# Performance work log

Hardware: AMD Instinct MI355X
Metric: run time of the kernel (lower is better)

The kernel has to match this reference:

```python
import jax, jax.numpy as jnp
import numpy as np

B_, T_, L_, M_, H_, F_ = 16, 2048, 128, 256, 512, 1024
EPS = 1e-5


def _init_reservoir(h, rng):
    # orthogonal matrix scaled inside the unit disk for a stable linear recurrence
    q, _ = np.linalg.qr(rng.standard_normal((h, h)).astype(np.float32))
    return jnp.asarray(0.95 * q, dtype=jnp.float32)


def setup_inputs() -> dict:
    key = jax.random.key(0)
    ks = jax.random.split(key, 8)
    rng = np.random.default_rng(0)
    s = lambda fan_in: 1.0 / np.sqrt(fan_in)
    return {
        "x": jax.random.normal(ks[0], (B_, T_, L_), dtype=jnp.float32),
        "We": jax.random.uniform(ks[1], (L_, M_), jnp.float32, -s(L_), s(L_)),
        "be": jnp.zeros((M_,), jnp.float32),
        "Wb": jax.random.uniform(ks[2], (M_, H_), jnp.float32, -s(M_), s(M_)),
        "A": _init_reservoir(H_, rng),
        "Wr": jax.random.uniform(ks[3], (L_, H_), jnp.float32, -s(L_), s(L_)),
        "br": jnp.zeros((H_,), jnp.float32),
        "ln_g": jnp.ones((H_,), jnp.float32),
        "ln_b": jnp.zeros((H_,), jnp.float32),
        "W1": jax.random.uniform(ks[4], (H_, F_), jnp.float32, -s(H_), s(H_)),
        "b1": jnp.zeros((F_,), jnp.float32),
        "W2": jax.random.uniform(ks[5], (F_, H_), jnp.float32, -s(F_), s(F_)),
        "b2": jnp.zeros((H_,), jnp.float32),
    }


def reference(x, We, be, Wb, A, Wr, br, ln_g, ln_b, W1, b1, W2, b2):
    # encoder + B projection, batched over all timesteps: [B,T,H]
    Bu = (x @ We + be) @ Wb

    # sequential linear recurrence h_t = h_{t-1} @ A + Bu_t, h_0 = Bu_0
    def step(h, bu_t):
        h = h @ A + bu_t
        return h, h

    h0 = jnp.zeros((x.shape[0], A.shape[0]), x.dtype)
    _, Hs = jax.lax.scan(step, h0, jnp.swapaxes(Bu, 0, 1))  # [T,B,H]
    H_seq = jnp.swapaxes(Hs, 0, 1)  # [B,T,H]

    # residual + layer norm
    z = H_seq + (x @ Wr + br)
    mu = jnp.mean(z, axis=-1, keepdims=True)
    var = jnp.mean(jnp.square(z - mu), axis=-1, keepdims=True)
    zn = (z - mu) * jax.lax.rsqrt(var + EPS) * ln_g + ln_b

    # MLP on last timestep
    h_last = zn[:, -1, :]
    out = jax.nn.relu(h_last @ W1 + b1) @ W2 + b2
    return out
```

## Files before the change

### kernel.cpp

```cpp
#include <hip/hip_runtime.h>

#define B_  16
#define T_  2048
#define L_  128
#define M_  256
#define H_  512
#define F_  1024
#define EPS 1e-5f

#define LDA_S 36
#define LDB_S 68
#define SMSZ (64 * LDA_S + 64 * LDB_S)

__device__ __forceinline__ float4 load_a4(const float* __restrict__ A,
                                          const float* __restrict__ Alast,
                                          int M, int lda, int amode,
                                          int gr, int gk) {
    float4 av = make_float4(0.f, 0.f, 0.f, 0.f);
    if (gr < M) {
        const float* p;
        if (amode == 1)
            p = A + (long)((gr & 15) * T_ + (T_ - 1 - (gr >> 4))) * L_ + gk;
        else if (amode == 2)
            p = A + (long)(((gr >> 4) << 5) + 16 + (gr & 15)) * lda + gk;
        else if (amode == 3 && gr == M - 1)
            p = Alast + gk;
        else
            p = A + (long)gr * lda + gk;
        av = *(const float4*)p;
    }
    return av;
}

__device__ __forceinline__ void gemm_tile(
    float* sm,
    const float* __restrict__ A, const float* __restrict__ Alast,
    const float* __restrict__ Bm, const float* __restrict__ bias,
    const float* __restrict__ Add, float* __restrict__ C,
    int M, int K, int lda, int ldb, int ldc,
    int flags, int amode, int bx, int by)
{
    constexpr int BM = 32, BN = 64, BK = 64, TM = 2, TN = 4;
    float* As = sm;
    float* Bs = sm + BK * LDA_S;
    const int tid = threadIdx.x;
    const int tx = tid & 15;
    const int ty = tid >> 4;
    const int row0 = by * BM, col0 = bx * BN;

    float4 pa[2], pb[4];
#pragma unroll
    for (int t = 0; t < 2; ++t) {
        int f = tid + t * 256;
        pa[t] = load_a4(A, Alast, M, lda, amode, row0 + (f >> 4), (f & 15) * 4);
    }
#pragma unroll
    for (int t = 0; t < 4; ++t) {
        int f = tid + t * 256;
        pb[t] = *(const float4*)(Bm + (long)(f >> 4) * ldb + col0 + (f & 15) * 4);
    }

    float acc[TM][TN] = {};

    for (int k0 = 0; k0 < K; k0 += BK) {
        __syncthreads();
#pragma unroll
        for (int t = 0; t < 2; ++t) {
            int f = tid + t * 256;
            int arow = f >> 4, kk = (f & 15) * 4;
            As[(kk + 0) * LDA_S + arow] = pa[t].x;
            As[(kk + 1) * LDA_S + arow] = pa[t].y;
            As[(kk + 2) * LDA_S + arow] = pa[t].z;
            As[(kk + 3) * LDA_S + arow] = pa[t].w;
        }
#pragma unroll
        for (int t = 0; t < 4; ++t) {
            int f = tid + t * 256;
            *(float4*)&Bs[(f >> 4) * LDB_S + (f & 15) * 4] = pb[t];
        }
        __syncthreads();
        int kn = k0 + BK;
        if (kn < K) {
#pragma unroll
            for (int t = 0; t < 2; ++t) {
                int f = tid + t * 256;
                pa[t] = load_a4(A, Alast, M, lda, amode, row0 + (f >> 4), kn + (f & 15) * 4);
            }
#pragma unroll
            for (int t = 0; t < 4; ++t) {
                int f = tid + t * 256;
                pb[t] = *(const float4*)(Bm + (long)(kn + (f >> 4)) * ldb + col0 + (f & 15) * 4);
            }
        }
#pragma unroll
        for (int kk = 0; kk < BK; ++kk) {
            float ra[TM], rb[TN];
#pragma unroll
            for (int i = 0; i < TM; ++i) ra[i] = As[kk * LDA_S + ty * TM + i];
#pragma unroll
            for (int j = 0; j < TN; ++j) rb[j] = Bs[kk * LDB_S + tx * TN + j];
#pragma unroll
            for (int i = 0; i < TM; ++i)
#pragma unroll
                for (int j = 0; j < TN; ++j)
                    acc[i][j] = fmaf(ra[i], rb[j], acc[i][j]);
        }
    }

#pragma unroll
    for (int i = 0; i < TM; ++i) {
        int r = row0 + ty * TM + i;
        if (r >= M) continue;
#pragma unroll
        for (int j = 0; j < TN; ++j) {
            int c = col0 + tx * TN + j;
            float v = acc[i][j];
            if (flags & 1) v += bias[c];
            if (amode == 2) v += Add[(long)(((r >> 4) << 5) + (r & 15)) * ldc + c];
            C[(long)r * ldc + c] = v;
        }
    }
}

__global__ __launch_bounds__(256) void dual(
    const float* A, const float* Alast, const float* Bm, const float* bias,
    const float* Add, float* C, int M, int K, int lda, int ldb, int ldc,
    int flags, int amode, int nbxA, int nA,
    const float* SqL, const float* SqR, float* SqOut)
{
    __shared__ float sm[SMSZ];
    int j = blockIdx.x;
    if (j < nA)
        gemm_tile(sm, A, Alast, Bm, bias, Add, C, M, K, lda, ldb, ldc,
                  flags, amode, j % nbxA, j / nbxA);
    else {
        int s = j - nA;
        gemm_tile(sm, SqL, nullptr, SqR, nullptr, nullptr, SqOut,
                  H_, H_, H_, H_, H_, 0, 0, s % 8, s / 8);
    }
}

#define TLDA 20
#define TLDB 68
#define TSM (64 * TLDA + 64 * TLDB)

__device__ __forceinline__ float4 z_a4(const float* __restrict__ V1,
                                       const float* __restrict__ x,
                                       int b, int gk) {
    int seg = gk >> 9;
    if (seg < 3)
        return *(const float4*)(V1 + (long)((seg + 1) * 16 + b) * H_ + (gk & 511));
    return *(const float4*)(x + ((long)b * T_ + (T_ - 1)) * L_ + (gk - 1536));
}

__device__ __forceinline__ float4 z_b4(const float* __restrict__ P32,
                                       const float* __restrict__ P64,
                                       const float* __restrict__ P96,
                                       const float* __restrict__ Wr,
                                       int kr, int c) {
    const float* p;
    if (kr < 512)       p = P32 + (long)kr * H_;
    else if (kr < 1024) p = P64 + (long)(kr - 512) * H_;
    else if (kr < 1536) p = P96 + (long)(kr - 1024) * H_;
    else                p = Wr + (long)(kr - 1536) * H_;
    return *(const float4*)(p + c);
}

__global__ __launch_bounds__(256) void zpart(
    const float* __restrict__ V1, const float* __restrict__ x,
    const float* __restrict__ P32, const float* __restrict__ P64,
    const float* __restrict__ P96, const float* __restrict__ Wr,
    float* __restrict__ zp)
{
    __shared__ float sm[TSM];
    float* As = sm;
    float* Bs = sm + 64 * TLDA;
    const int tid = threadIdx.x;
    const int tx = tid & 15, ty = tid >> 4;
    const int kc = blockIdx.x >> 3;
    const int col0 = (blockIdx.x & 7) * 64;
    const int kOff = kc * 128;

    float4 pa, pb[4];
    pa = z_a4(V1, x, tid >> 4, kOff + (tid & 15) * 4);
#pragma unroll
    for (int t = 0; t < 4; ++t) {
        int f = tid + t * 256;
        pb[t] = z_b4(P32, P64, P96, Wr, kOff + (f >> 4), col0 + (f & 15) * 4);
    }

    float acc[4] = {};
    for (int k0 = kOff; k0 < kOff + 128; k0 += 64) {
        __syncthreads();
        {
            int arow = tid >> 4, kk = (tid & 15) * 4;
            As[(kk + 0) * TLDA + arow] = pa.x;
            As[(kk + 1) * TLDA + arow] = pa.y;
            As[(kk + 2) * TLDA + arow] = pa.z;
            As[(kk + 3) * TLDA + arow] = pa.w;
        }
#pragma unroll
        for (int t = 0; t < 4; ++t) {
            int f = tid + t * 256;
            *(float4*)&Bs[(f >> 4) * TLDB + (f & 15) * 4] = pb[t];
        }
        __syncthreads();
        int kn = k0 + 64;
        if (kn < kOff + 128) {
            pa = z_a4(V1, x, tid >> 4, kn + (tid & 15) * 4);
#pragma unroll
            for (int t = 0; t < 4; ++t) {
                int f = tid + t * 256;
                pb[t] = z_b4(P32, P64, P96, Wr, kn + (f >> 4), col0 + (f & 15) * 4);
            }
        }
#pragma unroll
        for (int kk = 0; kk < 64; ++kk) {
            float ra = As[kk * TLDA + ty];
            float4 rb = *(float4*)&Bs[kk * TLDB + tx * 4];
            acc[0] = fmaf(ra, rb.x, acc[0]);
            acc[1] = fmaf(ra, rb.y, acc[1]);
            acc[2] = fmaf(ra, rb.z, acc[2]);
            acc[3] = fmaf(ra, rb.w, acc[3]);
        }
    }

    float* dst = zp + (long)kc * 16 * H_ + (long)ty * H_ + col0 + tx * 4;
    *(float4*)dst = make_float4(acc[0], acc[1], acc[2], acc[3]);
}

__global__ __launch_bounds__(256) void mlp1z(
    const float* __restrict__ V1, const float* __restrict__ zp,
    const float* __restrict__ br, const float* __restrict__ lng,
    const float* __restrict__ lnb, const float* __restrict__ W1,
    const float* __restrict__ b1, float* __restrict__ hid)
{
    __shared__ float znL[16 * 512];
    __shared__ float Bs[64 * TLDB];
    const int tid = threadIdx.x;

    {
        const int r = tid >> 4;
        const int l = tid & 15;
        float4 zv[8];
        float s1 = 0.f, s2 = 0.f;
#pragma unroll
        for (int i = 0; i < 8; ++i) {
            int c = l * 4 + i * 64;
            float4 v = *(const float4*)(V1 + (long)r * H_ + c);
            float4 bb = *(const float4*)(br + c);
            v.x += bb.x; v.y += bb.y; v.z += bb.z; v.w += bb.w;
#pragma unroll
            for (int kc = 0; kc < 13; ++kc) {
                float4 p = *(const float4*)(zp + (long)kc * 16 * H_ + (long)r * H_ + c);
                v.x += p.x; v.y += p.y; v.z += p.z; v.w += p.w;
            }
            zv[i] = v;
            s1 += v.x + v.y + v.z + v.w;
            s2 += v.x * v.x + v.y * v.y + v.z * v.z + v.w * v.w;
        }
#pragma unroll
        for (int off = 1; off < 16; off <<= 1) {
            s1 += __shfl_xor(s1, off, 64);
            s2 += __shfl_xor(s2, off, 64);
        }
        float mu  = s1 * (1.0f / H_);
        float var = s2 * (1.0f / H_) - mu * mu;
        float rs  = rsqrtf(var + EPS);
#pragma unroll
        for (int i = 0; i < 8; ++i) {
            int c = l * 4 + i * 64;
            float4 g  = *(const float4*)(lng + c);
            float4 bt = *(const float4*)(lnb + c);
            float4 v  = zv[i];
            v.x = (v.x - mu) * rs * g.x + bt.x;
            v.y = (v.y - mu) * rs * g.y + bt.y;
            v.z = (v.z - mu) * rs * g.z + bt.z;
            v.w = (v.w - mu) * rs * g.w + bt.w;
            *(float4*)&znL[r * 512 + c] = v;
        }
    }
    __syncthreads();

    const int tx = tid & 15, ty = tid >> 4;
    const int col0 = blockIdx.x * 64;

    float4 pb[4];
#pragma unroll
    for (int t = 0; t < 4; ++t) {
        int f = tid + t * 256;
        pb[t] = *(const float4*)(W1 + (long)(f >> 4) * F_ + col0 + (f & 15) * 4);
    }
    float acc[4] = {};
    for (int k0 = 0; k0 < H_; k0 += 64) {
        __syncthreads();
#pragma unroll
        for (int t = 0; t < 4; ++t) {
            int f = tid + t * 256;
            *(float4*)&Bs[(f >> 4) * TLDB + (f & 15) * 4] = pb[t];
        }
        __syncthreads();
        int kn = k0 + 64;
        if (kn < H_) {
#pragma unroll
            for (int t = 0; t < 4; ++t) {
                int f = tid + t * 256;
                pb[t] = *(const float4*)(W1 + (long)(kn + (f >> 4)) * F_ + col0 + (f & 15) * 4);
            }
        }
#pragma unroll
        for (int kk = 0; kk < 64; ++kk) {
            float ra = znL[ty * 512 + k0 + kk];
            float4 rb = *(float4*)&Bs[kk * TLDB + tx * 4];
            acc[0] = fmaf(ra, rb.x, acc[0]);
            acc[1] = fmaf(ra, rb.y, acc[1]);
            acc[2] = fmaf(ra, rb.z, acc[2]);
            acc[3] = fmaf(ra, rb.w, acc[3]);
        }
    }
    int c = col0 + tx * 4;
    float4 v;
    v.x = fmaxf(acc[0] + b1[c + 0], 0.f);
    v.y = fmaxf(acc[1] + b1[c + 1], 0.f);
    v.z = fmaxf(acc[2] + b1[c + 2], 0.f);
    v.w = fmaxf(acc[3] + b1[c + 3], 0.f);
    *(float4*)(hid + (long)ty * F_ + c) = v;
}

__global__ __launch_bounds__(256) void mlp2k(
    const float* __restrict__ hid, const float* __restrict__ W2,
    const float* __restrict__ b2, float* __restrict__ out)
{
    __shared__ float sm[TSM];
    float* As = sm;
    float* Bs = sm + 64 * TLDA;
    const int tid = threadIdx.x;
    const int tx = tid & 15, ty = tid >> 4;
    const int col0 = blockIdx.x * 64;

    float4 pa, pb[4];
    pa = *(const float4*)(hid + (long)(tid >> 4) * F_ + (tid & 15) * 4);
#pragma unroll
    for (int t = 0; t < 4; ++t) {
        int f = tid + t * 256;
        pb[t] = *(const float4*)(W2 + (long)(f >> 4) * H_ + col0 + (f & 15) * 4);
    }

    float acc[4] = {};
    for (int k0 = 0; k0 < F_; k0 += 64) {
        __syncthreads();
        {
            int arow = tid >> 4, kk = (tid & 15) * 4;
            As[(kk + 0) * TLDA + arow] = pa.x;
            As[(kk + 1) * TLDA + arow] = pa.y;
            As[(kk + 2) * TLDA + arow] = pa.z;
            As[(kk + 3) * TLDA + arow] = pa.w;
        }
#pragma unroll
        for (int t = 0; t < 4; ++t) {
            int f = tid + t * 256;
            *(float4*)&Bs[(f >> 4) * TLDB + (f & 15) * 4] = pb[t];
        }
        __syncthreads();
        int kn = k0 + 64;
        if (kn < F_) {
            pa = *(const float4*)(hid + (long)(tid >> 4) * F_ + kn + (tid & 15) * 4);
#pragma unroll
            for (int t = 0; t < 4; ++t) {
                int f = tid + t * 256;
                pb[t] = *(const float4*)(W2 + (long)(kn + (f >> 4)) * H_ + col0 + (f & 15) * 4);
            }
        }
#pragma unroll
        for (int kk = 0; kk < 64; ++kk) {
            float ra = As[kk * TLDA + ty];
            float4 rb = *(float4*)&Bs[kk * TLDB + tx * 4];
            acc[0] = fmaf(ra, rb.x, acc[0]);
            acc[1] = fmaf(ra, rb.y, acc[1]);
            acc[2] = fmaf(ra, rb.z, acc[2]);
            acc[3] = fmaf(ra, rb.w, acc[3]);
        }
    }

    int c = col0 + tx * 4;
    float4 v;
    v.x = acc[0] + b2[c + 0];
    v.y = acc[1] + b2[c + 1];
    v.z = acc[2] + b2[c + 2];
    v.w = acc[3] + b2[c + 3];
    *(float4*)(out + (long)ty * H_ + c) = v;
}

extern "C" void kernel_launch(void* const* d_in, const int* in_sizes, int n_in,
                              void* d_out, int out_size, void* d_ws, size_t ws_size,
                              hipStream_t stream) {
    const float* x    = (const float*)d_in[0];
    const float* We   = (const float*)d_in[1];
    const float* be   = (const float*)d_in[2];
    const float* Wb   = (const float*)d_in[3];
    const float* Amat = (const float*)d_in[4];
    const float* Wr   = (const float*)d_in[5];
    const float* br   = (const float*)d_in[6];
    const float* lng  = (const float*)d_in[7];
    const float* lnb  = (const float*)d_in[8];
    const float* W1   = (const float*)d_in[9];
    const float* b1   = (const float*)d_in[10];
    const float* W2   = (const float*)d_in[11];
    const float* b2   = (const float*)d_in[12];
    float* out = (float*)d_out;

    float* ws  = (float*)d_ws;
    float* Wc  = ws;
    float* V0  = Wc + 129 * H_;
    float* V1  = V0 + 2048 * H_;
    float* P2  = V1 + 1024 * H_;
    float* P4  = P2 + H_ * H_;
    float* P8  = P4 + H_ * H_;
    float* P16 = P8 + H_ * H_;
    float* P32 = P16 + H_ * H_;
    float* P64 = P32 + H_ * H_;
    float* P96 = P64 + H_ * H_;
    float* hid = P96 + H_ * H_;
    float* zp  = hid + B_ * F_;

    dual<<<168, 256, 0, stream>>>(We, be, Wb, nullptr, nullptr, Wc,
                                  129, M_, M_, H_, H_, 0, 3, 8, 40,
                                  Amat, Amat, P2);
    dual<<<640, 256, 0, stream>>>(x, nullptr, Wc, Wc + 128 * H_, nullptr, V0,
                                  2048, L_, L_, H_, H_, 1, 1, 8, 512,
                                  P2, P2, P4);
    dual<<<384, 256, 0, stream>>>(V0, nullptr, Amat, nullptr, V0, V1,
                                  1024, H_, H_, H_, H_, 0, 2, 8, 256,
                                  P4, P4, P8);
    dual<<<256, 256, 0, stream>>>(V1, nullptr, P2, nullptr, V1, V0,
                                  512, H_, H_, H_, H_, 0, 2, 8, 128,
                                  P8, P8, P16);
    dual<<<192, 256, 0, stream>>>(V0, nullptr, P4, nullptr, V0, V1,
                                  256, H_, H_, H_, H_, 0, 2, 8, 64,
                                  P16, P16, P32);
    dual<<<160, 256, 0, stream>>>(V1, nullptr, P8, nullptr, V1, V0,
                                  128, H_, H_, H_, H_, 0, 2, 8, 32,
                                  P32, P32, P64);
    dual<<<144, 256, 0, stream>>>(V0, nullptr, P16, nullptr, V0, V1,
                                  64, H_, H_, H_, H_, 0, 2, 8, 16,
                                  P32, P64, P96);
    zpart<<<104, 256, 0, stream>>>(V1, x, P32, P64, P96, Wr, zp);
    mlp1z<<<16, 256, 0, stream>>>(V1, zp, br, lng, lnb, W1, b1, hid);
    mlp2k<<<8, 256, 0, stream>>>(hid, W2, b2, out);
}
```

Measured before the change: 326.9 us.

## Split-K the final MLP GEMMs across more blocks with a reduction kernel

The two MLP matmuls on the last timestep previously ran on 16 and 8 blocks with long K loops. Each is now split along K into 128-wide chunks, giving 64 blocks each. Partial sums go to workspace, and bias/ReLU is folded into the second GEMM's A-load. A small reduction kernel adds the partials and b2. This raises parallelism on a latency-bound tail, at the cost of an extra launch, redundant layernorm stats per block, and extra partial-sum traffic.

```diff
diff --git a/kernel.cpp b/kernel.cpp
--- a/kernel.cpp
+++ b/kernel.cpp
@@ -229,20 +229,24 @@
     *(float4*)dst = make_float4(acc[0], acc[1], acc[2], acc[3]);
 }
 
-__global__ __launch_bounds__(256) void mlp1z(
+__global__ __launch_bounds__(256) void zmlp1(
     const float* __restrict__ V1, const float* __restrict__ zp,
     const float* __restrict__ br, const float* __restrict__ lng,
     const float* __restrict__ lnb, const float* __restrict__ W1,
-    const float* __restrict__ b1, float* __restrict__ hid)
-{
-    __shared__ float znL[16 * 512];
+    float* __restrict__ h1p)
+{
+    __shared__ float znS[16][132];
     __shared__ float Bs[64 * TLDB];
     const int tid = threadIdx.x;
+    const int kc   = blockIdx.x >> 4;
+    const int col0 = (blockIdx.x & 15) * 64;
+    const int kOff = kc * 128;
 
     {
         const int r = tid >> 4;
         const int l = tid & 15;
-        float4 zv[8];
+        float4 keep0 = make_float4(0.f, 0.f, 0.f, 0.f);
+        float4 keep1 = make_float4(0.f, 0.f, 0.f, 0.f);
         float s1 = 0.f, s2 = 0.f;
 #pragma unroll
         for (int i = 0; i < 8; ++i) {
@@ -251,13 +255,14 @@
             float4 bb = *(const float4*)(br + c);
             v.x += bb.x; v.y += bb.y; v.z += bb.z; v.w += bb.w;
 #pragma unroll
-            for (int kc = 0; kc < 13; ++kc) {
-                float4 p = *(const float4*)(zp + (long)kc * 16 * H_ + (long)r * H_ + c);
-                v.x += p.x; v.y += p.y; v.z += p.z; v.w += p.w;
-            }
-            zv[i] = v;
+            for (int p = 0; p < 13; ++p) {
+                float4 q = *(const float4*)(zp + (long)p * 16 * H_ + (long)r * H_ + c);
+                v.x += q.x; v.y += q.y; v.z += q.z; v.w += q.w;
+            }
             s1 += v.x + v.y + v.z + v.w;
             s2 += v.x * v.x + v.y * v.y + v.z * v.z + v.w * v.w;
+            if (i == (kc << 1))     keep0 = v;
+            if (i == (kc << 1) + 1) keep1 = v;
         }
 #pragma unroll
         for (int off = 1; off < 16; off <<= 1) {
@@ -267,32 +272,37 @@
         float mu  = s1 * (1.0f / H_);
         float var = s2 * (1.0f / H_) - mu * mu;
         float rs  = rsqrtf(var + EPS);
-#pragma unroll
-        for (int i = 0; i < 8; ++i) {
-            int c = l * 4 + i * 64;
-            float4 g  = *(const float4*)(lng + c);
-            float4 bt = *(const float4*)(lnb + c);
-            float4 v  = zv[i];
-            v.x = (v.x - mu) * rs * g.x + bt.x;
-            v.y = (v.y - mu) * rs * g.y + bt.y;
-            v.z = (v.z - mu) * rs * g.z + bt.z;
-            v.w = (v.w - mu) * rs * g.w + bt.w;
-            *(float4*)&znL[r * 512 + c] = v;
-        }
-    }
-    __syncthreads();
+
+        int c0 = kOff + l * 4;
+        float4 g0 = *(const float4*)(lng + c0);
+        float4 t0 = *(const float4*)(lnb + c0);
+        keep0.x = (keep0.x - mu) * rs * g0.x + t0.x;
+        keep0.y = (keep0.y - mu) * rs * g0.y + t0.y;
+        keep0.z = (keep0.z - mu) * rs * g0.z + t0.z;
+        keep0.w = (keep0.w - mu) * rs * g0.w + t0.w;
+        int c1 = c0 + 64;
+        float4 g1 = *(const float4*)(lng + c1);
+        float4 t1 = *(const float4*)(lnb + c1);
+        keep1.x = (keep1.x - mu) * rs * g1.x + t1.x;
+        keep1.y = (keep1.y - mu) * rs * g1.y + t1.y;
+        keep1.z = (keep1.z - mu) * rs * g1.z + t1.z;
+        keep1.w = (keep1.w - mu) * rs * g1.w + t1.w;
+
+        znS[r][l * 4 + 0] = keep0.x; znS[r][l * 4 + 1] = keep0.y;
+        znS[r][l * 4 + 2] = keep0.z; znS[r][l * 4 + 3] = keep0.w;
+        znS[r][64 + l * 4 + 0] = keep1.x; znS[r][64 + l * 4 + 1] = keep1.y;
+        znS[r][64 + l * 4 + 2] = keep1.z; znS[r][64 + l * 4 + 3] = keep1.w;
+    }
 
     const int tx = tid & 15, ty = tid >> 4;
-    const int col0 = blockIdx.x * 64;
-
     float4 pb[4];
 #pragma unroll
     for (int t = 0; t < 4; ++t) {
         int f = tid + t * 256;
-        pb[t] = *(const float4*)(W1 + (long)(f >> 4) * F_ + col0 + (f & 15) * 4);
+        pb[t] = *(const float4*)(W1 + (long)(kOff + (f >> 4)) * F_ + col0 + (f & 15) * 4);
     }
     float acc[4] = {};
-    for (int k0 = 0; k0 < H_; k0 += 64) {
+    for (int k0 = 0; k0 < 128; k0 += 64) {
         __syncthreads();
 #pragma unroll
         for (int t = 0; t < 4; ++t) {
@@ -300,17 +310,16 @@
             *(float4*)&Bs[(f >> 4) * TLDB + (f & 15) * 4] = pb[t];
         }
         __syncthreads();
-        int kn = k0 + 64;
-        if (kn < H_) {
+        if (k0 == 0) {
 #pragma unroll
             for (int t = 0; t < 4; ++t) {
                 int f = tid + t * 256;
-                pb[t] = *(const float4*)(W1 + (long)(kn + (f >> 4)) * F_ + col0 + (f & 15) * 4);
+                pb[t] = *(const float4*)(W1 + (long)(kOff + 64 + (f >> 4)) * F_ + col0 + (f & 15) * 4);
             }
         }
 #pragma unroll
         for (int kk = 0; kk < 64; ++kk) {
-            float ra = znL[ty * 512 + k0 + kk];
+            float ra = znS[ty][k0 + kk];
             float4 rb = *(float4*)&Bs[kk * TLDB + tx * 4];
             acc[0] = fmaf(ra, rb.x, acc[0]);
             acc[1] = fmaf(ra, rb.y, acc[1]);
@@ -318,36 +327,47 @@
             acc[3] = fmaf(ra, rb.w, acc[3]);
         }
     }
-    int c = col0 + tx * 4;
-    float4 v;
-    v.x = fmaxf(acc[0] + b1[c + 0], 0.f);
-    v.y = fmaxf(acc[1] + b1[c + 1], 0.f);
-    v.z = fmaxf(acc[2] + b1[c + 2], 0.f);
-    v.w = fmaxf(acc[3] + b1[c + 3], 0.f);
-    *(float4*)(hid + (long)ty * F_ + c) = v;
-}
-
-__global__ __launch_bounds__(256) void mlp2k(
-    const float* __restrict__ hid, const float* __restrict__ W2,
-    const float* __restrict__ b2, float* __restrict__ out)
+    float* dst = h1p + (long)kc * 16 * F_ + (long)ty * F_ + col0 + tx * 4;
+    *(float4*)dst = make_float4(acc[0], acc[1], acc[2], acc[3]);
+}
+
+__device__ __forceinline__ float4 hid_a4(const float* __restrict__ h1p,
+                                         const float* __restrict__ b1,
+                                         int b, int gk) {
+    float4 v = *(const float4*)(b1 + gk);
+#pragma unroll
+    for (int p = 0; p < 4; ++p) {
+        float4 q = *(const float4*)(h1p + (long)p * 16 * F_ + (long)b * F_ + gk);
+        v.x += q.x; v.y += q.y; v.z += q.z; v.w += q.w;
+    }
+    v.x = fmaxf(v.x, 0.f); v.y = fmaxf(v.y, 0.f);
+    v.z = fmaxf(v.z, 0.f); v.w = fmaxf(v.w, 0.f);
+    return v;
+}
+
+__global__ __launch_bounds__(256) void hmlp2(
+    const float* __restrict__ h1p, const float* __restrict__ b1,
+    const float* __restrict__ W2, float* __restrict__ op)
 {
     __shared__ float sm[TSM];
     float* As = sm;
     float* Bs = sm + 64 * TLDA;
     const int tid = threadIdx.x;
     const int tx = tid & 15, ty = tid >> 4;
-    const int col0 = blockIdx.x * 64;
+    const int kc = blockIdx.x >> 3;
+    const int col0 = (blockIdx.x & 7) * 64;
+    const int kOff = kc * 128;
 
     float4 pa, pb[4];
-    pa = *(const float4*)(hid + (long)(tid >> 4) * F_ + (tid & 15) * 4);
+    pa = hid_a4(h1p, b1, tid >> 4, kOff + (tid & 15) * 4);
 #pragma unroll
     for (int t = 0; t < 4; ++t) {
         int f = tid + t * 256;
-        pb[t] = *(const float4*)(W2 + (long)(f >> 4) * H_ + col0 + (f & 15) * 4);
+        pb[t] = *(const float4*)(W2 + (long)(kOff + (f >> 4)) * H_ + col0 + (f & 15) * 4);
     }
 
     float acc[4] = {};
-    for (int k0 = 0; k0 < F_; k0 += 64) {
+    for (int k0 = kOff; k0 < kOff + 128; k0 += 64) {
         __syncthreads();
         {
             int arow = tid >> 4, kk = (tid & 15) * 4;
@@ -363,8 +383,8 @@
         }
         __syncthreads();
         int kn = k0 + 64;
-        if (kn < F_) {
-            pa = *(const float4*)(hid + (long)(tid >> 4) * F_ + kn + (tid & 15) * 4);
+        if (kn < kOff + 128) {
+            pa = hid_a4(h1p, b1, tid >> 4, kn + (tid & 15) * 4);
 #pragma unroll
             for (int t = 0; t < 4; ++t) {
                 int f = tid + t * 256;
@@ -382,13 +402,21 @@
         }
     }
 
-    int c = col0 + tx * 4;
-    float4 v;
-    v.x = acc[0] + b2[c + 0];
-    v.y = acc[1] + b2[c + 1];
-    v.z = acc[2] + b2[c + 2];
-    v.w = acc[3] + b2[c + 3];
-    *(float4*)(out + (long)ty * H_ + c) = v;
+    float* dst = op + (long)kc * 16 * H_ + (long)ty * H_ + col0 + tx * 4;
+    *(float4*)dst = make_float4(acc[0], acc[1], acc[2], acc[3]);
+}
+
+__global__ __launch_bounds__(256) void ored(
+    const float* __restrict__ op, const float* __restrict__ b2,
+    float* __restrict__ out)
+{
+    int b = blockIdx.x >> 1;
+    int c = (blockIdx.x & 1) * 256 + threadIdx.x;
+    float s = b2[c];
+#pragma unroll
+    for (int kc = 0; kc < 8; ++kc)
+        s += op[(long)kc * 16 * H_ + (long)b * H_ + c];
+    out[(long)b * H_ + c] = s;
 }
 
 extern "C" void kernel_launch(void* const* d_in, const int* in_sizes, int n_in,
@@ -420,8 +448,9 @@
     float* P32 = P16 + H_ * H_;
     float* P64 = P32 + H_ * H_;
     float* P96 = P64 + H_ * H_;
-    float* hid = P96 + H_ * H_;
-    float* zp  = hid + B_ * F_;
+    float* zp  = P96 + H_ * H_;
+    float* h1p = zp + 13 * B_ * H_;
+    float* op  = h1p + 4 * B_ * F_;
 
     dual<<<168, 256, 0, stream>>>(We, be, Wb, nullptr, nullptr, Wc,
                                   129, M_, M_, H_, H_, 0, 3, 8, 40,
@@ -445,6 +474,7 @@
                                   64, H_, H_, H_, H_, 0, 2, 8, 16,
                                   P32, P64, P96);
     zpart<<<104, 256, 0, stream>>>(V1, x, P32, P64, P96, Wr, zp);
-    mlp1z<<<16, 256, 0, stream>>>(V1, zp, br, lng, lnb, W1, b1, hid);
-    mlp2k<<<8, 256, 0, stream>>>(hid, W2, b2, out);
-}
+    zmlp1<<<64, 256, 0, stream>>>(V1, zp, br, lng, lnb, W1, h1p);
+    hmlp2<<<64, 256, 0, stream>>>(h1p, b1, W2, op);
+    ored<<<32, 256, 0, stream>>>(op, b2, out);
+}
```

Measured after the change: 291.5 us. -10.9%, faster.
